# Kernel optimization log

Measured on AMD Instinct MI355X. Metric: run time of the kernel, lower is better.

## Reference

```python
import jax, jax.numpy as jnp
import numpy as np

N, T, D, M = 16, 4096, 256, 512


def setup_inputs() -> dict:
    key = jax.random.key(0)
    k1, k2 = jax.random.split(key)
    x = jax.random.normal(k1, (N, T, D), dtype=jnp.float32)
    # codebook initialized like the module: uniform(-1/M, 1/M) then row-normalized
    init_bound = 1.0 / M
    emb = jax.random.uniform(k2, (M, D), dtype=jnp.float32, minval=-init_bound, maxval=init_bound)
    emb = emb / (jnp.linalg.norm(emb, axis=1, keepdims=True) + 1e-4)
    return {"x": x, "embedding": emb}


def reference(x, embedding):
    sg = jax.lax.stop_gradient
    # L2_distance: distances computed against the row-normalized codebook,
    # but the gather uses the raw (unnormalized) codebook.
    emb_norm = embedding / (jnp.linalg.norm(embedding, axis=1, keepdims=True) + 1e-4)
    x_flat = sg(x).reshape(-1, D)  # (N*T, D), detached in torch
    distances = (jnp.sum(emb_norm ** 2, axis=1)[None, :]
                 + jnp.sum(x_flat ** 2, axis=1, keepdims=True)
                 - 2.0 * (x_flat @ emb_norm.T))  # (N*T, M)
    indices = jnp.argmin(distances, axis=-1)  # (N*T,)
    encodings = jax.nn.one_hot(indices, M, dtype=jnp.float32)  # (N*T, M)
    quantized = embedding[indices].reshape(x.shape)  # (N, T, D)

    commitment_loss = jnp.mean((sg(x) - quantized) ** 2)
    quantized_ = x + sg(quantized - x)           # straight-through
    quantized_ = (quantized_ + quantized) / 2.0  # averaged with raw-grad path

    avg_probs = jnp.mean(encodings, axis=0)  # (M,)
    perplexity = jnp.exp(-jnp.sum(avg_probs * jnp.log(avg_probs + 1e-10)))
    return quantized_, commitment_loss, perplexity
```

## Files before the change

kernel.cpp:

```cpp
#include <hip/hip_runtime.h>
#include <hip/hip_bf16.h>


typedef _Float16 half8_t __attribute__((ext_vector_type(8)));
typedef _Float16 half4_t __attribute__((ext_vector_type(4)));
typedef float f32x4 __attribute__((ext_vector_type(4)));

static constexpr int kRows = 65536;
static constexpr int kD = 256;
static constexpr int kM = 512;
static constexpr int kBM = 64;

typedef const unsigned int __attribute__((address_space(1)))* gas_t;
typedef unsigned int __attribute__((address_space(3)))* las_t;

__global__ void vq_prep(const float* __restrict__ emb, _Float16* __restrict__ swz,
                        float* __restrict__ bias, unsigned int* __restrict__ hist,
                        float* __restrict__ loss) {
    const int j = blockIdx.x;
    const int lane = threadIdx.x;
    float4 v = ((const float4*)(emb + j * kD))[lane];
    float ss = v.x * v.x + v.y * v.y + v.z * v.z + v.w * v.w;
    #pragma unroll
    for (int off = 32; off > 0; off >>= 1) ss += __shfl_xor(ss, off);
    const float scale = 1.0f / (sqrtf(ss) + 1e-4f);
    if (lane == 0) bias[j] = 0.5f * ss * scale * scale;
    half4_t h;
    h[0] = (_Float16)(v.x * scale);
    h[1] = (_Float16)(v.y * scale);
    h[2] = (_Float16)(v.z * scale);
    h[3] = (_Float16)(v.w * scale);
    const int k0 = lane * 4;
    const int ko = k0 >> 5;
    const int qd = (k0 >> 3) & 3;
    const int jj = k0 & 7;
    const int off_h = (j >> 4) * 4096 + ko * 512 + (qd * 16 + (j & 15)) * 8 + jj;
    *(half4_t*)(swz + off_h) = h;
    if (j == 0) {
        for (int b = lane; b < kM; b += 64) hist[b] = 0u;
        if (lane == 0) loss[0] = 0.0f;
    }
}

__global__ __launch_bounds__(128, 2) void vq_main(
    const float* __restrict__ x, const float* __restrict__ emb,
    const _Float16* __restrict__ bswz, const float* __restrict__ bias,
    unsigned int* __restrict__ hist, float* __restrict__ loss_accum,
    float* __restrict__ out) {
    __shared__ _Float16 bb[64 * kD];
    __shared__ float lbias[kM];
    __shared__ unsigned int lhist[kM];
    __shared__ int lidx[kBM];
    __shared__ float lred[2];

    const int t = threadIdx.x;
    const int row0 = blockIdx.x * kBM;
    const int wave = t >> 6;
    const int lane = t & 63;
    const int qd = lane >> 4;
    const int ln = lane & 15;

    #pragma unroll
    for (int b = t; b < kM; b += 128) { lhist[b] = 0u; lbias[b] = bias[b]; }

    half8_t a[2][8];
    #pragma unroll
    for (int s = 0; s < 2; ++s) {
        const float* xr = x + (size_t)(row0 + wave * 32 + s * 16 + ln) * kD + qd * 8;
        #pragma unroll
        for (int ko = 0; ko < 8; ++ko) {
            const float4 v0 = *(const float4*)(xr + ko * 32);
            const float4 v1 = *(const float4*)(xr + ko * 32 + 4);
            half8_t h;
            h[0] = (_Float16)v0.x; h[1] = (_Float16)v0.y;
            h[2] = (_Float16)v0.z; h[3] = (_Float16)v0.w;
            h[4] = (_Float16)v1.x; h[5] = (_Float16)v1.y;
            h[6] = (_Float16)v1.z; h[7] = (_Float16)v1.w;
            a[s][ko] = h;
        }
    }

    float bv[2][4] = {{-1e30f, -1e30f, -1e30f, -1e30f}, {-1e30f, -1e30f, -1e30f, -1e30f}};
    int bi[2][4] = {{0, 0, 0, 0}, {0, 0, 0, 0}};
    #pragma unroll 1
    for (int st = 0; st < 8; ++st) {
        __syncthreads();
        {
            const _Float16* src = bswz + (size_t)st * 16384 + wave * 512 + lane * 8;
            _Float16* dst = bb + wave * 512 + lane * 8;
            #pragma unroll
            for (int i = 0; i < 16; ++i)
                __builtin_amdgcn_global_load_lds((gas_t)(const void*)(src + i * 1024),
                                                 (las_t)(void*)(dst + i * 1024), 16, 0, 0);
        }
        __syncthreads();
        #pragma unroll
        for (int sg = 0; sg < 4; ++sg) {
            const int c = st * 64 + sg * 16 + ln;
            const float bbias = lbias[c];
            f32x4 acc0 = {-bbias, -bbias, -bbias, -bbias};
            f32x4 acc1 = {-bbias, -bbias, -bbias, -bbias};
            const half8_t* bp = (const half8_t*)bb + sg * 512 + lane;
            #pragma unroll
            for (int ko = 0; ko < 8; ++ko) {
                const half8_t bf = bp[ko * 64];
                acc0 = __builtin_amdgcn_mfma_f32_16x16x32_f16(a[0][ko], bf, acc0, 0, 0, 0);
                acc1 = __builtin_amdgcn_mfma_f32_16x16x32_f16(a[1][ko], bf, acc1, 0, 0, 0);
            }
            #pragma unroll
            for (int r = 0; r < 4; ++r) {
                if (acc0[r] > bv[0][r]) { bv[0][r] = acc0[r]; bi[0][r] = c; }
                if (acc1[r] > bv[1][r]) { bv[1][r] = acc1[r]; bi[1][r] = c; }
            }
        }
    }

    #pragma unroll
    for (int s = 0; s < 2; ++s) {
        #pragma unroll
        for (int r = 0; r < 4; ++r) {
            #pragma unroll
            for (int off = 1; off < 16; off <<= 1) {
                const float ov = __shfl_xor(bv[s][r], off);
                const int oi = __shfl_xor(bi[s][r], off);
                if (ov > bv[s][r] || (ov == bv[s][r] && oi < bi[s][r])) { bv[s][r] = ov; bi[s][r] = oi; }
            }
            if (ln == 0) {
                const int row = wave * 32 + s * 16 + qd * 4 + r;
                lidx[row] = bi[s][r];
                atomicAdd(&lhist[bi[s][r]], 1u);
            }
        }
    }
    __syncthreads();

    float lsum = 0.0f;
    {
        const float* xg = x + (size_t)row0 * kD;
        float* og = out + (size_t)row0 * kD;
        #pragma unroll 8
        for (int i = 0; i < 32; ++i) {
            const int g = t * 4 + i * 512;
            const int r = g >> 8;
            const float4 xv = *(const float4*)(xg + g);
            const int idx = lidx[r];
            const float4 q = *(const float4*)(emb + (size_t)idx * kD + (g & 255));
            const float d0 = xv.x - q.x, d1 = xv.y - q.y, d2 = xv.z - q.z, d3 = xv.w - q.w;
            lsum += d0 * d0 + d1 * d1 + d2 * d2 + d3 * d3;
            float4 o;
            o.x = ((xv.x + (q.x - xv.x)) + q.x) * 0.5f;
            o.y = ((xv.y + (q.y - xv.y)) + q.y) * 0.5f;
            o.z = ((xv.z + (q.z - xv.z)) + q.z) * 0.5f;
            o.w = ((xv.w + (q.w - xv.w)) + q.w) * 0.5f;
            *(float4*)&og[g] = o;
        }
    }
    #pragma unroll
    for (int off = 32; off > 0; off >>= 1) lsum += __shfl_xor(lsum, off);
    if (lane == 0) lred[wave] = lsum;
    __syncthreads();
    if (t == 0) atomicAdd(loss_accum, lred[0] + lred[1]);

    #pragma unroll
    for (int b = t; b < kM; b += 128) {
        const unsigned int h = lhist[b];
        if (h) atomicAdd(&hist[b], h);
    }
}

__global__ void vq_final(const unsigned int* __restrict__ hist,
                         const float* __restrict__ loss_accum,
                         float* __restrict__ out) {
    const int t = threadIdx.x;
    __shared__ float sr[4];
    float s = 0.0f;
    for (int b = t; b < kM; b += 256) {
        const float p = (float)hist[b] * (1.0f / 65536.0f);
        s += p * logf(p + 1e-10f);
    }
    #pragma unroll
    for (int off = 32; off > 0; off >>= 1) s += __shfl_xor(s, off);
    if ((t & 63) == 0) sr[t >> 6] = s;
    __syncthreads();
    if (t == 0) {
        const float tot = sr[0] + sr[1] + sr[2] + sr[3];
        out[16777217] = expf(-tot);
        out[16777216] = loss_accum[0] * (1.0f / 16777216.0f);
    }
}

extern "C" void kernel_launch(void* const* d_in, const int* in_sizes, int n_in,
                              void* d_out, int out_size, void* d_ws, size_t ws_size,
                              hipStream_t stream) {
    const float* x = (const float*)d_in[0];
    const float* emb = (const float*)d_in[1];
    char* ws = (char*)d_ws;
    _Float16* bswz = (_Float16*)ws;
    float* bias = (float*)(ws + 262144);
    unsigned int* hist = (unsigned int*)(ws + 262144 + 2048);
    float* loss = (float*)(ws + 262144 + 4096);
    float* out = (float*)d_out;

    vq_prep<<<kM, 64, 0, stream>>>(emb, bswz, bias, hist, loss);
    vq_main<<<kRows / kBM, 128, 0, stream>>>(x, emb, bswz, bias, hist, loss, out);
    vq_final<<<1, 256, 0, stream>>>(hist, loss, out);
}
```

Before: 147.8 us.

## Double-buffer codebook stages in LDS and use 128-row blocks with four waves

The main kernel now processes 128 rows per block with 256 threads and double-buffers the codebook slices in shared memory. The next slice is prefetched with async global-to-LDS loads while MFMAs run on the current one, with explicit waitcnt and barriers in place of the two syncthreads per stage. This is meant to hide codebook load latency and halve codebook reloads per row. In exchange LDS use per block doubles to about 64KB+, which may limit occupancy, and the hand-written waitcnt counts must match the number of loads issued.

After: 142.9 us. 3.3% less time.

```diff
diff --git a/kernel.cpp b/kernel.cpp
--- a/kernel.cpp
+++ b/kernel.cpp
@@ -9,7 +9,7 @@
 static constexpr int kRows = 65536;
 static constexpr int kD = 256;
 static constexpr int kM = 512;
-static constexpr int kBM = 64;
+static constexpr int kBM = 128;
 
 typedef const unsigned int __attribute__((address_space(1)))* gas_t;
 typedef unsigned int __attribute__((address_space(3)))* las_t;
@@ -42,16 +42,16 @@
     }
 }
 
-__global__ __launch_bounds__(128, 2) void vq_main(
+__global__ __launch_bounds__(256, 2) void vq_main(
     const float* __restrict__ x, const float* __restrict__ emb,
     const _Float16* __restrict__ bswz, const float* __restrict__ bias,
     unsigned int* __restrict__ hist, float* __restrict__ loss_accum,
     float* __restrict__ out) {
-    __shared__ _Float16 bb[64 * kD];
+    __shared__ _Float16 bb[2][64 * kD];
     __shared__ float lbias[kM];
     __shared__ unsigned int lhist[kM];
     __shared__ int lidx[kBM];
-    __shared__ float lred[2];
+    __shared__ float lred[4];
 
     const int t = threadIdx.x;
     const int row0 = blockIdx.x * kBM;
@@ -60,8 +60,8 @@
     const int qd = lane >> 4;
     const int ln = lane & 15;
 
-    #pragma unroll
-    for (int b = t; b < kM; b += 128) { lhist[b] = 0u; lbias[b] = bias[b]; }
+    lhist[t] = 0u;          lhist[t + 256] = 0u;
+    lbias[t] = bias[t];     lbias[t + 256] = bias[t + 256];
 
     half8_t a[2][8];
     #pragma unroll
@@ -80,27 +80,34 @@
         }
     }
 
+    auto stage_load = [&](int st, int buf) {
+        const _Float16* src = bswz + (size_t)st * 16384 + t * 8;
+        _Float16* dst = &bb[buf][0] + t * 8;
+        #pragma unroll
+        for (int i = 0; i < 8; ++i)
+            __builtin_amdgcn_global_load_lds((gas_t)(const void*)(src + i * 2048),
+                                             (las_t)(void*)(dst + i * 2048), 16, 0, 0);
+    };
+
+    stage_load(0, 0);
+
     float bv[2][4] = {{-1e30f, -1e30f, -1e30f, -1e30f}, {-1e30f, -1e30f, -1e30f, -1e30f}};
     int bi[2][4] = {{0, 0, 0, 0}, {0, 0, 0, 0}};
     #pragma unroll 1
     for (int st = 0; st < 8; ++st) {
-        __syncthreads();
-        {
-            const _Float16* src = bswz + (size_t)st * 16384 + wave * 512 + lane * 8;
-            _Float16* dst = bb + wave * 512 + lane * 8;
-            #pragma unroll
-            for (int i = 0; i < 16; ++i)
-                __builtin_amdgcn_global_load_lds((gas_t)(const void*)(src + i * 1024),
-                                                 (las_t)(void*)(dst + i * 1024), 16, 0, 0);
-        }
-        __syncthreads();
+        if (st < 7) stage_load(st + 1, (st + 1) & 1);
+        if (st == 0)      __asm__ __volatile__("s_waitcnt vmcnt(8) lgkmcnt(0)\ns_barrier" ::: "memory");
+        else if (st < 7)  __asm__ __volatile__("s_waitcnt vmcnt(8)\ns_barrier" ::: "memory");
+        else              __asm__ __volatile__("s_waitcnt vmcnt(0)\ns_barrier" ::: "memory");
+
+        const _Float16* bbase = &bb[st & 1][0];
         #pragma unroll
         for (int sg = 0; sg < 4; ++sg) {
             const int c = st * 64 + sg * 16 + ln;
             const float bbias = lbias[c];
             f32x4 acc0 = {-bbias, -bbias, -bbias, -bbias};
             f32x4 acc1 = {-bbias, -bbias, -bbias, -bbias};
-            const half8_t* bp = (const half8_t*)bb + sg * 512 + lane;
+            const half8_t* bp = (const half8_t*)bbase + sg * 512 + lane;
             #pragma unroll
             for (int ko = 0; ko < 8; ++ko) {
                 const half8_t bf = bp[ko * 64];
@@ -113,6 +120,7 @@
                 if (acc1[r] > bv[1][r]) { bv[1][r] = acc1[r]; bi[1][r] = c; }
             }
         }
+        if (st < 7) __asm__ __volatile__("s_barrier" ::: "memory");
     }
 
     #pragma unroll
@@ -140,7 +148,7 @@
         float* og = out + (size_t)row0 * kD;
         #pragma unroll 8
         for (int i = 0; i < 32; ++i) {
-            const int g = t * 4 + i * 512;
+            const int g = t * 4 + i * 1024;
             const int r = g >> 8;
             const float4 xv = *(const float4*)(xg + g);
             const int idx = lidx[r];
@@ -159,13 +167,12 @@
     for (int off = 32; off > 0; off >>= 1) lsum += __shfl_xor(lsum, off);
     if (lane == 0) lred[wave] = lsum;
     __syncthreads();
-    if (t == 0) atomicAdd(loss_accum, lred[0] + lred[1]);
-
-    #pragma unroll
-    for (int b = t; b < kM; b += 128) {
-        const unsigned int h = lhist[b];
-        if (h) atomicAdd(&hist[b], h);
-    }
+    if (t == 0) atomicAdd(loss_accum, lred[0] + lred[1] + lred[2] + lred[3]);
+
+    const unsigned int h0 = lhist[t];
+    if (h0) atomicAdd(&hist[t], h0);
+    const unsigned int h1 = lhist[t + 256];
+    if (h1) atomicAdd(&hist[t + 256], h1);
 }
 
 __global__ void vq_final(const unsigned int* __restrict__ hist,
@@ -202,6 +209,6 @@
     float* out = (float*)d_out;
 
     vq_prep<<<kM, 64, 0, stream>>>(emb, bswz, bias, hist, loss);
-    vq_main<<<kRows / kBM, 128, 0, stream>>>(x, emb, bswz, bias, hist, loss, out);
+    vq_main<<<kRows / kBM, 256, 0, stream>>>(x, emb, bswz, bias, hist, loss, out);
     vq_final<<<1, 256, 0, stream>>>(hist, loss, out);
 }
```

## Double-buffer codebook staging and split epilogue into separate kernel

Applied to the files above, without the earlier changes.

The argmin kernel now streams the swizzled codebook in 32-code stages through two LDS buffers, issuing the next stage's async global-to-LDS loads before computing on the current one, with manual waitcnt and barriers. The gather, loss and output write move to a new 256-thread epilogue kernel that reads indices from workspace. This aims to overlap codebook loads with MFMA work and give the memory-bound epilogue its own occupancy. In exchange it adds an extra launch, an index round trip through global memory, and a second full read of x.

After: 167.4 us. 1.13x slower.

```diff
diff --git a/kernel.cpp b/kernel.cpp
--- a/kernel.cpp
+++ b/kernel.cpp
@@ -9,7 +9,6 @@
 static constexpr int kRows = 65536;
 static constexpr int kD = 256;
 static constexpr int kM = 512;
-static constexpr int kBM = 64;
 
 typedef const unsigned int __attribute__((address_space(1)))* gas_t;
 typedef unsigned int __attribute__((address_space(3)))* las_t;
@@ -42,19 +41,16 @@
     }
 }
 
-__global__ __launch_bounds__(128, 2) void vq_main(
-    const float* __restrict__ x, const float* __restrict__ emb,
-    const _Float16* __restrict__ bswz, const float* __restrict__ bias,
-    unsigned int* __restrict__ hist, float* __restrict__ loss_accum,
-    float* __restrict__ out) {
-    __shared__ _Float16 bb[64 * kD];
+__global__ __launch_bounds__(128, 2) void vq_argmin(
+    const float* __restrict__ x, const _Float16* __restrict__ bswz,
+    const float* __restrict__ bias, unsigned int* __restrict__ hist,
+    int* __restrict__ idx_out) {
+    __shared__ _Float16 bb[2][32 * kD];
     __shared__ float lbias[kM];
     __shared__ unsigned int lhist[kM];
-    __shared__ int lidx[kBM];
-    __shared__ float lred[2];
 
     const int t = threadIdx.x;
-    const int row0 = blockIdx.x * kBM;
+    const int row0 = blockIdx.x * 64;
     const int wave = t >> 6;
     const int lane = t & 63;
     const int qd = lane >> 4;
@@ -80,27 +76,34 @@
         }
     }
 
+    auto stage_load = [&](int st, int buf) {
+        const _Float16* src = bswz + (size_t)st * 8192 + t * 8;
+        _Float16* dst = &bb[buf][0] + t * 8;
+        #pragma unroll
+        for (int i = 0; i < 8; ++i)
+            __builtin_amdgcn_global_load_lds((gas_t)(const void*)(src + i * 1024),
+                                             (las_t)(void*)(dst + i * 1024), 16, 0, 0);
+    };
+
+    stage_load(0, 0);
+
     float bv[2][4] = {{-1e30f, -1e30f, -1e30f, -1e30f}, {-1e30f, -1e30f, -1e30f, -1e30f}};
     int bi[2][4] = {{0, 0, 0, 0}, {0, 0, 0, 0}};
     #pragma unroll 1
-    for (int st = 0; st < 8; ++st) {
-        __syncthreads();
-        {
-            const _Float16* src = bswz + (size_t)st * 16384 + wave * 512 + lane * 8;
-            _Float16* dst = bb + wave * 512 + lane * 8;
-            #pragma unroll
-            for (int i = 0; i < 16; ++i)
-                __builtin_amdgcn_global_load_lds((gas_t)(const void*)(src + i * 1024),
-                                                 (las_t)(void*)(dst + i * 1024), 16, 0, 0);
-        }
-        __syncthreads();
-        #pragma unroll
-        for (int sg = 0; sg < 4; ++sg) {
-            const int c = st * 64 + sg * 16 + ln;
+    for (int st = 0; st < 16; ++st) {
+        if (st < 15) stage_load(st + 1, (st + 1) & 1);
+        if (st == 0)       __asm__ __volatile__("s_waitcnt vmcnt(8) lgkmcnt(0)\ns_barrier" ::: "memory");
+        else if (st < 15)  __asm__ __volatile__("s_waitcnt vmcnt(8)\ns_barrier" ::: "memory");
+        else               __asm__ __volatile__("s_waitcnt vmcnt(0)\ns_barrier" ::: "memory");
+
+        const _Float16* bbase = &bb[st & 1][0];
+        #pragma unroll
+        for (int sg = 0; sg < 2; ++sg) {
+            const int c = st * 32 + sg * 16 + ln;
             const float bbias = lbias[c];
             f32x4 acc0 = {-bbias, -bbias, -bbias, -bbias};
             f32x4 acc1 = {-bbias, -bbias, -bbias, -bbias};
-            const half8_t* bp = (const half8_t*)bb + sg * 512 + lane;
+            const half8_t* bp = (const half8_t*)bbase + sg * 512 + lane;
             #pragma unroll
             for (int ko = 0; ko < 8; ++ko) {
                 const half8_t bf = bp[ko * 64];
@@ -113,6 +116,7 @@
                 if (acc1[r] > bv[1][r]) { bv[1][r] = acc1[r]; bi[1][r] = c; }
             }
         }
+        if (st < 15) __asm__ __volatile__("s_barrier" ::: "memory");
     }
 
     #pragma unroll
@@ -126,46 +130,54 @@
                 if (ov > bv[s][r] || (ov == bv[s][r] && oi < bi[s][r])) { bv[s][r] = ov; bi[s][r] = oi; }
             }
             if (ln == 0) {
-                const int row = wave * 32 + s * 16 + qd * 4 + r;
-                lidx[row] = bi[s][r];
+                idx_out[row0 + wave * 32 + s * 16 + qd * 4 + r] = bi[s][r];
                 atomicAdd(&lhist[bi[s][r]], 1u);
             }
         }
     }
     __syncthreads();
-
-    float lsum = 0.0f;
-    {
-        const float* xg = x + (size_t)row0 * kD;
-        float* og = out + (size_t)row0 * kD;
-        #pragma unroll 8
-        for (int i = 0; i < 32; ++i) {
-            const int g = t * 4 + i * 512;
-            const int r = g >> 8;
-            const float4 xv = *(const float4*)(xg + g);
-            const int idx = lidx[r];
-            const float4 q = *(const float4*)(emb + (size_t)idx * kD + (g & 255));
-            const float d0 = xv.x - q.x, d1 = xv.y - q.y, d2 = xv.z - q.z, d3 = xv.w - q.w;
-            lsum += d0 * d0 + d1 * d1 + d2 * d2 + d3 * d3;
-            float4 o;
-            o.x = ((xv.x + (q.x - xv.x)) + q.x) * 0.5f;
-            o.y = ((xv.y + (q.y - xv.y)) + q.y) * 0.5f;
-            o.z = ((xv.z + (q.z - xv.z)) + q.z) * 0.5f;
-            o.w = ((xv.w + (q.w - xv.w)) + q.w) * 0.5f;
-            *(float4*)&og[g] = o;
-        }
-    }
-    #pragma unroll
-    for (int off = 32; off > 0; off >>= 1) lsum += __shfl_xor(lsum, off);
-    if (lane == 0) lred[wave] = lsum;
-    __syncthreads();
-    if (t == 0) atomicAdd(loss_accum, lred[0] + lred[1]);
 
     #pragma unroll
     for (int b = t; b < kM; b += 128) {
         const unsigned int h = lhist[b];
         if (h) atomicAdd(&hist[b], h);
     }
+}
+
+__global__ __launch_bounds__(256) void vq_epilogue(
+    const float* __restrict__ x, const float* __restrict__ emb,
+    const int* __restrict__ idx, float* __restrict__ loss_accum,
+    float* __restrict__ out) {
+    __shared__ int li[64];
+    __shared__ float lred[4];
+    const int t = threadIdx.x;
+    const int row0 = blockIdx.x * 64;
+    if (t < 64) li[t] = idx[row0 + t];
+    __syncthreads();
+
+    float lsum = 0.0f;
+    const float* xg = x + (size_t)row0 * kD;
+    float* og = out + (size_t)row0 * kD;
+    #pragma unroll
+    for (int i = 0; i < 16; ++i) {
+        const int g = t * 4 + i * 1024;
+        const int r = g >> 8;
+        const float4 xv = *(const float4*)(xg + g);
+        const float4 q = *(const float4*)(emb + (size_t)li[r] * kD + (g & 255));
+        const float d0 = xv.x - q.x, d1 = xv.y - q.y, d2 = xv.z - q.z, d3 = xv.w - q.w;
+        lsum += d0 * d0 + d1 * d1 + d2 * d2 + d3 * d3;
+        float4 o;
+        o.x = ((xv.x + (q.x - xv.x)) + q.x) * 0.5f;
+        o.y = ((xv.y + (q.y - xv.y)) + q.y) * 0.5f;
+        o.z = ((xv.z + (q.z - xv.z)) + q.z) * 0.5f;
+        o.w = ((xv.w + (q.w - xv.w)) + q.w) * 0.5f;
+        *(float4*)&og[g] = o;
+    }
+    #pragma unroll
+    for (int off = 32; off > 0; off >>= 1) lsum += __shfl_xor(lsum, off);
+    if ((t & 63) == 0) lred[t >> 6] = lsum;
+    __syncthreads();
+    if (t == 0) atomicAdd(loss_accum, lred[0] + lred[1] + lred[2] + lred[3]);
 }
 
 __global__ void vq_final(const unsigned int* __restrict__ hist,
@@ -199,9 +211,11 @@
     float* bias = (float*)(ws + 262144);
     unsigned int* hist = (unsigned int*)(ws + 262144 + 2048);
     float* loss = (float*)(ws + 262144 + 4096);
+    int* idx = (int*)(ws + 262144 + 4096 + 64);
     float* out = (float*)d_out;
 
     vq_prep<<<kM, 64, 0, stream>>>(emb, bswz, bias, hist, loss);
-    vq_main<<<kRows / kBM, 128, 0, stream>>>(x, emb, bswz, bias, hist, loss, out);
+    vq_argmin<<<kRows / 64, 128, 0, stream>>>(x, bswz, bias, hist, idx);
+    vq_epilogue<<<kRows / 64, 256, 0, stream>>>(x, emb, idx, loss, out);
     vq_final<<<1, 256, 0, stream>>>(hist, loss, out);
 }
```
